# Kernel optimization log

Measured on AMD Instinct MI355X. Metric: run time of the kernel, lower is better.

The kernel has to match this reference:

```python
import jax, jax.numpy as jnp
import numpy as np


def setup_inputs() -> dict:
    key = jax.random.key(0)
    k1, k2, k3, k4, k5 = jax.random.split(key, 5)
    n_mol, n_atm, d_feat, n_props = 128, 64, 384, 64
    n_ref = n_mol * n_atm  # 8192 reference atoms (flattened)
    # element labels in {1,2,3,4} (e.g. H,C,N,O); all atoms nondummy (Z>0)
    Z_ref = jax.random.randint(k1, (n_mol, n_atm), 1, 5)
    Z = jax.random.randint(k2, (n_mol, n_atm), 1, 5)
    # descriptors, scaled so the poly kernel K^expK stays O(1)
    scale = 1.0 / np.sqrt(d_feat).astype(np.float32)
    X_ref = jax.random.normal(k3, (n_ref, d_feat), jnp.float32) * scale
    desc = jax.random.normal(k4, (n_mol, n_atm, d_feat), jnp.float32) * scale
    Alpha = jax.random.normal(k5, (n_props, n_ref), jnp.float32)
    return {"Alpha": Alpha, "X_ref": X_ref, "desc": desc,
            "Z_ref": Z_ref, "Z": Z, "expK": 2}


def reference(Alpha, X_ref, desc, Z_ref, Z, expK):
    # Faithful dense formulation of the per-element gather/matmul/scatter:
    # y[p, j] = sum_i Alpha[p, i] * (X_ref[i] . X_in[j])^expK * [Z_ref[i] == Z[j]]
    # Each query atom j belongs to exactly one element, so the masked dense
    # kernel reproduces the grouped computation exactly (same flat ordering
    # as torch's molecule-major concatenation).
    d_feat = X_ref.shape[-1]
    X_in = desc.reshape(-1, d_feat)                      # [N_in, d]
    K = jnp.power(X_ref @ X_in.T, expK)                  # [N_ref, N_in]
    mask = Z_ref.reshape(-1)[:, None] == Z.reshape(-1)[None, :]
    y = Alpha @ jnp.where(mask, K, jnp.float32(0.0))     # [n_props, N_in]
    return y
```

## Files before the change

### kernel.cpp

```cpp
#include <hip/hip_runtime.h>
#include <hip/hip_bf16.h>
#include <stdint.h>


typedef __attribute__((ext_vector_type(8))) short bf16x8;
typedef __attribute__((ext_vector_type(4))) float f32x4;
typedef __attribute__((ext_vector_type(4))) unsigned int u32x4;

#define DFEAT  384
#define NREF   8192
#define NIN    8192
#define NPROPS 64
#define BJ 128
#define BI 128
#define BK 64
#define KSTEPS (DFEAT / BK)
#define CAP    8704
#define NSTRIP (CAP / BJ)

__device__ __forceinline__ void gload_lds16(const void* g, void* l) {
  __builtin_amdgcn_global_load_lds(
      (const __attribute__((address_space(1))) void*)g,
      (__attribute__((address_space(3))) void*)l,
      16, 0, 0);
}

__device__ __forceinline__ unsigned short bfbits(float f) {
  __hip_bfloat16 h = __float2bfloat16(f);
  return __builtin_bit_cast(unsigned short, h);
}

__device__ __forceinline__ float pwr(float s, int expK) {
  if (expK == 2) return s * s;
  float r = 1.0f;
  for (int e = 0; e < expK; ++e) r *= s;
  return r;
}

__global__ __launch_bounds__(256) void partition2_kernel(
    const int* __restrict__ Za, const int* __restrict__ Zb,
    int* __restrict__ perma, int* __restrict__ permb,
    int* __restrict__ goffa, int* __restrict__ goffb) {
  const int* Zin = blockIdx.x ? Zb : Za;
  int* perm = blockIdx.x ? permb : perma;
  int* goff = blockIdx.x ? goffb : goffa;

  __shared__ int cnt[256][4];
  __shared__ int gstart[4];
  __shared__ int gtot[4];
  const int t = threadIdx.x;
  const int base = t * 32;

  int c[4] = {0, 0, 0, 0};
  int zloc[32];
  #pragma unroll
  for (int e = 0; e < 32; ++e) {
    zloc[e] = (Zin[base + e] - 1) & 3;
    ++c[zloc[e]];
  }
  #pragma unroll
  for (int b = 0; b < 4; ++b) cnt[t][b] = c[b];
  __syncthreads();

  const int w = t >> 6, l = t & 63;
  {
    int v0 = cnt[4 * l + 0][w], v1 = cnt[4 * l + 1][w];
    int v2 = cnt[4 * l + 2][w], v3 = cnt[4 * l + 3][w];
    int s = v0 + v1 + v2 + v3;
    int inc = s;
    #pragma unroll
    for (int d = 1; d < 64; d <<= 1) {
      int o = __shfl_up(inc, d, 64);
      if (l >= d) inc += o;
    }
    const int excl = inc - s;
    cnt[4 * l + 0][w] = excl;
    cnt[4 * l + 1][w] = excl + v0;
    cnt[4 * l + 2][w] = excl + v0 + v1;
    cnt[4 * l + 3][w] = excl + v0 + v1 + v2;
    if (l == 63) gtot[w] = inc;
  }
  __syncthreads();

  if (t == 0) {
    int off = 0;
    #pragma unroll
    for (int b = 0; b < 4; ++b) {
      gstart[b] = off; goff[b] = off;
      off += ((gtot[b] + 127) >> 7) << 7;
    }
    goff[4] = off;
  }
  __syncthreads();

  for (int s = t; s < CAP; s += 256) perm[s] = -1;
  __syncthreads();

  int pos[4];
  #pragma unroll
  for (int b = 0; b < 4; ++b) pos[b] = gstart[b] + cnt[t][b];
  #pragma unroll
  for (int e = 0; e < 32; ++e) {
    const int z = zloc[e];
    perm[pos[z]++] = base + e;
  }
}

#define XSEC (CAP * (DFEAT / 4) / 256)
__global__ void gather_all(const float* __restrict__ Xr_in,
                           const float* __restrict__ Xi_in,
                           const float* __restrict__ Al_in,
                           const int* __restrict__ perm_i,
                           const int* __restrict__ perm_j,
                           __hip_bfloat16* __restrict__ Xr_g,
                           __hip_bfloat16* __restrict__ Xi_g,
                           __hip_bfloat16* __restrict__ Ab_g) {
  const int b = blockIdx.x;
  if (b < 2 * XSEC) {
    const bool isA = (b < XSEC);
    const float* in = isA ? Xr_in : Xi_in;
    const int* perm = isA ? perm_i : perm_j;
    __hip_bfloat16* out = isA ? Xr_g : Xi_g;
    const int idx = (isA ? b : b - XSEC) * 256 + threadIdx.x;
    const int per_row = DFEAT / 4;
    const int slot = idx / per_row;
    const int c4 = (idx % per_row) * 4;
    const int src = perm[slot];
    ushort4 o = make_ushort4(0, 0, 0, 0);
    if (src >= 0) {
      float4 v = *reinterpret_cast<const float4*>(in + (size_t)src * DFEAT + c4);
      o.x = bfbits(v.x); o.y = bfbits(v.y); o.z = bfbits(v.z); o.w = bfbits(v.w);
    }
    *reinterpret_cast<ushort4*>(out + (size_t)slot * DFEAT + c4) = o;
  } else {
    const int t = (b - 2 * XSEC) * 256 + threadIdx.x;
    const int per_row = CAP / 4;
    const int p  = t / per_row;
    const int c4 = t % per_row;
    const int blk = c4 >> 3;
    const int g   = c4 & 7;
    const int l4g = g >> 1;
    const int eh  = g & 1;
    ushort4 o;
    unsigned short* op = &o.x;
    #pragma unroll
    for (int r = 0; r < 4; ++r) {
      const int slot = blk * 32 + eh * 16 + l4g * 4 + r;
      const int src = perm_i[slot];
      op[r] = (src >= 0) ? bfbits(Al_in[(size_t)p * NREF + src]) : (unsigned short)0;
    }
    *reinterpret_cast<ushort4*>(Ab_g + (size_t)p * CAP + blk * 32 + l4g * 8 + eh * 4) = o;
  }
}

__global__ void reduce_scatter(const float* __restrict__ partial,
                               const int* __restrict__ permj,
                               float* __restrict__ out, int nsplit) {
  const int idx = blockIdx.x * blockDim.x + threadIdx.x;
  const int p = idx / CAP;
  const int slot = idx % CAP;
  const int dst = permj[slot];
  if (dst < 0) return;
  float s = 0.f;
  for (int sp = 0; sp < nsplit; ++sp)
    s += partial[(size_t)sp * NPROPS * CAP + (size_t)p * CAP + slot];
  out[(size_t)p * NIN + dst] = s;
}

__global__ __launch_bounds__(256, 2) void fused_poly_kernel(
    const __hip_bfloat16* __restrict__ Xr,
    const __hip_bfloat16* __restrict__ Xi,
    const __hip_bfloat16* __restrict__ Abp,
    const int* __restrict__ ioff,
    const int* __restrict__ joff,
    const int* __restrict__ expKp,
    float* __restrict__ partial,
    int nsplit, int chunk)
{
  const int flat = blockIdx.x;
  const int newflat = (flat & 7) * chunk + (flat >> 3);
  const int strip = newflat / nsplit;
  const int split = newflat % nsplit;
  const int j0 = strip * BJ;

  if (j0 >= joff[4]) return;

  int grp = 0;
  grp += (j0 >= joff[1]);
  grp += (j0 >= joff[2]);
  grp += (j0 >= joff[3]);
  const int ibase = ioff[grp];
  const int ntiles_g = (ioff[grp + 1] - ibase) / BI;

  const int tb = ntiles_g / nsplit;
  const int rem = ntiles_g % nsplit;
  const int ntiles = tb + (split < rem ? 1 : 0);
  const int tile_begin = split * tb + (split < rem ? split : rem);

  const int tid  = threadIdx.x;
  const int wid  = tid >> 6;
  const int lane = tid & 63;
  const int l15  = lane & 15;
  const int l4   = lane >> 4;
  const int s7   = l15 & 7;
  const int wi   = wid >> 1;
  const int wj   = wid & 1;

  __shared__ alignas(16) __hip_bfloat16 lA[2][BI * BK];
  __shared__ alignas(16) __hip_bfloat16 lB[2][BJ * BK];

  const int expK = *expKp;

  const int srow = lane >> 3;
  const int scol = ((lane & 7) ^ srow) * 8;

  auto stage = [&](int buf, int i0s, int kks) {
    #pragma unroll
    for (int q = 0; q < 4; ++q) {
      const int c = wid * 4 + q;
      const int grow = c * 8 + srow;
      const size_t gc = (size_t)kks * BK + scol;
      gload_lds16(Xr + (size_t)(i0s + grow) * DFEAT + gc, &lA[buf][c * 512]);
      gload_lds16(Xi + (size_t)(j0  + grow) * DFEAT + gc, &lB[buf][c * 512]);
    }
  };

  f32x4 accO[4][4];
  #pragma unroll
  for (int a = 0; a < 4; ++a)
    #pragma unroll
    for (int n = 0; n < 4; ++n)
      accO[a][n] = (f32x4){0.f, 0.f, 0.f, 0.f};

  if (ntiles > 0) {
    int cur = 0;
    stage(0, ibase + tile_begin * BI, 0);

    for (int t = 0; t < ntiles; ++t) {
      const int i0 = ibase + (tile_begin + t) * BI;

      f32x4 acc[4][4];
      #pragma unroll
      for (int m = 0; m < 4; ++m)
        #pragma unroll
        for (int n = 0; n < 4; ++n)
          acc[m][n] = (f32x4){0.f, 0.f, 0.f, 0.f};

      for (int kk = 0; kk < KSTEPS; ++kk) {
        bool staged = true;
        if (kk < KSTEPS - 1) {
          stage(cur ^ 1, i0, kk + 1);
        } else if (t < ntiles - 1) {
          stage(cur ^ 1, i0 + BI, 0);
        } else {
          staged = false;
        }
        if (staged) asm volatile("s_waitcnt vmcnt(8)" ::: "memory");
        else        asm volatile("s_waitcnt vmcnt(0)" ::: "memory");
        __builtin_amdgcn_s_barrier();

        __builtin_amdgcn_s_setprio(1);
        #pragma unroll
        for (int kap = 0; kap < 2; ++kap) {
          bf16x8 aF[4], bF[4];
          #pragma unroll
          for (int m = 0; m < 4; ++m) {
            const int rA = wi * 64 + m * 16 + l15;
            aF[m] = *reinterpret_cast<const bf16x8*>(
                (char*)(&lA[cur][0]) + rA * 128 + (((kap * 4 + l4) ^ s7) << 4));
          }
          #pragma unroll
          for (int n = 0; n < 4; ++n) {
            const int rB = wj * 64 + n * 16 + l15;
            bF[n] = *reinterpret_cast<const bf16x8*>(
                (char*)(&lB[cur][0]) + rB * 128 + (((kap * 4 + l4) ^ s7) << 4));
          }
          #pragma unroll
          for (int m = 0; m < 4; ++m)
            #pragma unroll
            for (int n = 0; n < 4; ++n)
              acc[m][n] = __builtin_amdgcn_mfma_f32_16x16x32_bf16(
                  aF[m], bF[n], acc[m][n], 0, 0, 0);
        }
        __builtin_amdgcn_s_setprio(0);
        asm volatile("s_waitcnt lgkmcnt(0)" ::: "memory");
        __builtin_amdgcn_s_barrier();
        cur ^= 1;
      }

      bf16x8 aP[2][4];
      #pragma unroll
      for (int ks = 0; ks < 2; ++ks)
        #pragma unroll
        for (int a = 0; a < 4; ++a)
          aP[ks][a] = *reinterpret_cast<const bf16x8*>(
              Abp + (size_t)(a * 16 + l15) * CAP + i0 + wi * 64 + ks * 32 + l4 * 8);

      uint32_t lov[4][4], hiv[4][4];
      #pragma unroll
      for (int m = 0; m < 4; ++m) {
        #pragma unroll
        for (int n = 0; n < 4; ++n) {
          const float p0 = pwr(acc[m][n][0], expK);
          const float p1 = pwr(acc[m][n][1], expK);
          const float p2 = pwr(acc[m][n][2], expK);
          const float p3 = pwr(acc[m][n][3], expK);
          lov[m][n] = (uint32_t)bfbits(p0) | ((uint32_t)bfbits(p1) << 16);
          hiv[m][n] = (uint32_t)bfbits(p2) | ((uint32_t)bfbits(p3) << 16);
        }
      }

      __builtin_amdgcn_s_setprio(1);
      #pragma unroll
      for (int ks = 0; ks < 2; ++ks) {
        #pragma unroll
        for (int n = 0; n < 4; ++n) {
          u32x4 tw;
          tw[0] = lov[2 * ks][n];
          tw[1] = hiv[2 * ks][n];
          tw[2] = lov[2 * ks + 1][n];
          tw[3] = hiv[2 * ks + 1][n];
          const bf16x8 bP = __builtin_bit_cast(bf16x8, tw);
          #pragma unroll
          for (int a = 0; a < 4; ++a)
            accO[a][n] = __builtin_amdgcn_mfma_f32_16x16x32_bf16(
                aP[ks][a], bP, accO[a][n], 0, 0, 0);
        }
      }
      __builtin_amdgcn_s_setprio(0);
    }
  }

  float* rb = (float*)lA;
  if (wi == 1) {
    #pragma unroll
    for (int a = 0; a < 4; ++a)
      #pragma unroll
      for (int n = 0; n < 4; ++n)
        #pragma unroll
        for (int r = 0; r < 4; ++r)
          rb[wj * 4096 + (a * 16 + l4 * 4 + r) * 64 + n * 16 + l15] =
              accO[a][n][r];
  }
  __syncthreads();
  if (wi == 0) {
    float* po = partial + (size_t)split * NPROPS * CAP;
    #pragma unroll
    for (int a = 0; a < 4; ++a)
      #pragma unroll
      for (int n = 0; n < 4; ++n)
        #pragma unroll
        for (int r = 0; r < 4; ++r) {
          const int p = a * 16 + l4 * 4 + r;
          const int jl = wj * 64 + n * 16 + l15;
          po[(size_t)p * CAP + j0 + jl] =
              accO[a][n][r] + rb[wj * 4096 + p * 64 + n * 16 + l15];
        }
  }
}

extern "C" void kernel_launch(void* const* d_in, const int* in_sizes, int n_in,
                              void* d_out, int out_size, void* d_ws, size_t ws_size,
                              hipStream_t stream) {
  (void)in_sizes; (void)n_in; (void)out_size;
  const float* Alpha = (const float*)d_in[0];
  const float* X_ref = (const float*)d_in[1];
  const float* desc  = (const float*)d_in[2];
  const int*   Z_ref = (const int*)d_in[3];
  const int*   Z     = (const int*)d_in[4];
  const int*   expK  = (const int*)d_in[5];
  float* out = (float*)d_out;

  char* ws = (char*)d_ws;
  size_t off = 0;
  auto alloc = [&](size_t b) { void* p = ws + off; off = (off + b + 255) & ~255ULL; return p; };

  int* perm_i = (int*)alloc(CAP * 4);
  int* perm_j = (int*)alloc(CAP * 4);
  int* ioff   = (int*)alloc(8 * 4);
  int* joff   = (int*)alloc(8 * 4);
  __hip_bfloat16* Xr_g = (__hip_bfloat16*)alloc((size_t)CAP * DFEAT * 2);
  __hip_bfloat16* Xi_g = (__hip_bfloat16*)alloc((size_t)CAP * DFEAT * 2);
  __hip_bfloat16* Ab_g = (__hip_bfloat16*)alloc((size_t)NPROPS * CAP * 2);

  int nsplit = 8;
  while (nsplit > 1 && off + (size_t)nsplit * NPROPS * CAP * 4 > ws_size) nsplit >>= 1;
  float* partial = (float*)alloc((size_t)nsplit * NPROPS * CAP * 4);

  partition2_kernel<<<dim3(2), 256, 0, stream>>>(
      Z_ref, Z, perm_i, perm_j, ioff, joff);

  gather_all<<<dim3(2 * XSEC + NPROPS * (CAP / 4) / 256), 256, 0, stream>>>(
      X_ref, desc, Alpha, perm_i, perm_j, Xr_g, Xi_g, Ab_g);

  const int grid = NSTRIP * nsplit;
  fused_poly_kernel<<<dim3(grid), 256, 0, stream>>>(
      Xr_g, Xi_g, Ab_g, ioff, joff, expK, partial, nsplit, grid / 8);

  reduce_scatter<<<dim3(NPROPS * CAP / 256), 256, 0, stream>>>(
      partial, perm_j, out, nsplit);
}
```

Before: 77.67 us.

## Drop LDS staging and load MFMA operands directly from global memory

```diff
diff --git a/kernel.cpp b/kernel.cpp
--- a/kernel.cpp
+++ b/kernel.cpp
@@ -13,17 +13,9 @@
 #define NPROPS 64
 #define BJ 128
 #define BI 128
-#define BK 64
-#define KSTEPS (DFEAT / BK)
+#define KSTEPS 6
 #define CAP    8704
 #define NSTRIP (CAP / BJ)
-
-__device__ __forceinline__ void gload_lds16(const void* g, void* l) {
-  __builtin_amdgcn_global_load_lds(
-      (const __attribute__((address_space(1))) void*)g,
-      (__attribute__((address_space(3))) void*)l,
-      16, 0, 0);
-}
 
 __device__ __forceinline__ unsigned short bfbits(float f) {
   __hip_bfloat16 h = __float2bfloat16(f);
@@ -167,7 +159,7 @@
   out[(size_t)p * NIN + dst] = s;
 }
 
-__global__ __launch_bounds__(256, 2) void fused_poly_kernel(
+__global__ __launch_bounds__(256, 4) void fused_poly_kernel(
     const __hip_bfloat16* __restrict__ Xr,
     const __hip_bfloat16* __restrict__ Xi,
     const __hip_bfloat16* __restrict__ Abp,
@@ -182,7 +174,6 @@
   const int strip = newflat / nsplit;
   const int split = newflat % nsplit;
   const int j0 = strip * BJ;
-
   if (j0 >= joff[4]) return;
 
   int grp = 0;
@@ -191,7 +182,6 @@
   grp += (j0 >= joff[3]);
   const int ibase = ioff[grp];
   const int ntiles_g = (ioff[grp + 1] - ibase) / BI;
-
   const int tb = ntiles_g / nsplit;
   const int rem = ntiles_g % nsplit;
   const int ntiles = tb + (split < rem ? 1 : 0);
@@ -202,90 +192,54 @@
   const int lane = tid & 63;
   const int l15  = lane & 15;
   const int l4   = lane >> 4;
-  const int s7   = l15 & 7;
-  const int wi   = wid >> 1;
-  const int wj   = wid & 1;
-
-  __shared__ alignas(16) __hip_bfloat16 lA[2][BI * BK];
-  __shared__ alignas(16) __hip_bfloat16 lB[2][BJ * BK];
+  const int jw   = j0 + wid * 32;
 
   const int expK = *expKp;
 
-  const int srow = lane >> 3;
-  const int scol = ((lane & 7) ^ srow) * 8;
-
-  auto stage = [&](int buf, int i0s, int kks) {
-    #pragma unroll
-    for (int q = 0; q < 4; ++q) {
-      const int c = wid * 4 + q;
-      const int grow = c * 8 + srow;
-      const size_t gc = (size_t)kks * BK + scol;
-      gload_lds16(Xr + (size_t)(i0s + grow) * DFEAT + gc, &lA[buf][c * 512]);
-      gload_lds16(Xi + (size_t)(j0  + grow) * DFEAT + gc, &lB[buf][c * 512]);
-    }
-  };
-
-  f32x4 accO[4][4];
+  const __hip_bfloat16* xiB = Xi + (size_t)(jw + l15) * DFEAT + l4 * 8;
+
+  f32x4 accO[4][2];
   #pragma unroll
   for (int a = 0; a < 4; ++a)
     #pragma unroll
-    for (int n = 0; n < 4; ++n)
+    for (int n = 0; n < 2; ++n)
       accO[a][n] = (f32x4){0.f, 0.f, 0.f, 0.f};
 
-  if (ntiles > 0) {
-    int cur = 0;
-    stage(0, ibase + tile_begin * BI, 0);
-
-    for (int t = 0; t < ntiles; ++t) {
-      const int i0 = ibase + (tile_begin + t) * BI;
-
-      f32x4 acc[4][4];
+  #pragma unroll 1
+  for (int t = 0; t < ntiles; ++t) {
+    const int i0 = ibase + (tile_begin + t) * BI;
+
+    #pragma unroll 1
+    for (int h = 0; h < 2; ++h) {
+      const __hip_bfloat16* xrA =
+          Xr + (size_t)(i0 + h * 64 + l15) * DFEAT + l4 * 8;
+
+      f32x4 acc[4][2];
       #pragma unroll
       for (int m = 0; m < 4; ++m)
         #pragma unroll
-        for (int n = 0; n < 4; ++n)
+        for (int n = 0; n < 2; ++n)
           acc[m][n] = (f32x4){0.f, 0.f, 0.f, 0.f};
 
+      #pragma unroll
       for (int kk = 0; kk < KSTEPS; ++kk) {
-        bool staged = true;
-        if (kk < KSTEPS - 1) {
-          stage(cur ^ 1, i0, kk + 1);
-        } else if (t < ntiles - 1) {
-          stage(cur ^ 1, i0 + BI, 0);
-        } else {
-          staged = false;
-        }
-        if (staged) asm volatile("s_waitcnt vmcnt(8)" ::: "memory");
-        else        asm volatile("s_waitcnt vmcnt(0)" ::: "memory");
-        __builtin_amdgcn_s_barrier();
-
-        __builtin_amdgcn_s_setprio(1);
         #pragma unroll
         for (int kap = 0; kap < 2; ++kap) {
-          bf16x8 aF[4], bF[4];
+          const int co = kk * 64 + kap * 32;
+          bf16x8 aF[4], bF[2];
           #pragma unroll
-          for (int m = 0; m < 4; ++m) {
-            const int rA = wi * 64 + m * 16 + l15;
-            aF[m] = *reinterpret_cast<const bf16x8*>(
-                (char*)(&lA[cur][0]) + rA * 128 + (((kap * 4 + l4) ^ s7) << 4));
-          }
+          for (int m = 0; m < 4; ++m)
+            aF[m] = *reinterpret_cast<const bf16x8*>(xrA + m * (16 * DFEAT) + co);
           #pragma unroll
-          for (int n = 0; n < 4; ++n) {
-            const int rB = wj * 64 + n * 16 + l15;
-            bF[n] = *reinterpret_cast<const bf16x8*>(
-                (char*)(&lB[cur][0]) + rB * 128 + (((kap * 4 + l4) ^ s7) << 4));
-          }
+          for (int n = 0; n < 2; ++n)
+            bF[n] = *reinterpret_cast<const bf16x8*>(xiB + n * (16 * DFEAT) + co);
           #pragma unroll
           for (int m = 0; m < 4; ++m)
             #pragma unroll
-            for (int n = 0; n < 4; ++n)
+            for (int n = 0; n < 2; ++n)
               acc[m][n] = __builtin_amdgcn_mfma_f32_16x16x32_bf16(
                   aF[m], bF[n], acc[m][n], 0, 0, 0);
         }
-        __builtin_amdgcn_s_setprio(0);
-        asm volatile("s_waitcnt lgkmcnt(0)" ::: "memory");
-        __builtin_amdgcn_s_barrier();
-        cur ^= 1;
       }
 
       bf16x8 aP[2][4];
@@ -294,13 +248,13 @@
         #pragma unroll
         for (int a = 0; a < 4; ++a)
           aP[ks][a] = *reinterpret_cast<const bf16x8*>(
-              Abp + (size_t)(a * 16 + l15) * CAP + i0 + wi * 64 + ks * 32 + l4 * 8);
-
-      uint32_t lov[4][4], hiv[4][4];
+              Abp + (size_t)(a * 16 + l15) * CAP + i0 + h * 64 + ks * 32 + l4 * 8);
+
+      uint32_t lov[4][2], hiv[4][2];
       #pragma unroll
       for (int m = 0; m < 4; ++m) {
         #pragma unroll
-        for (int n = 0; n < 4; ++n) {
+        for (int n = 0; n < 2; ++n) {
           const float p0 = pwr(acc[m][n][0], expK);
           const float p1 = pwr(acc[m][n][1], expK);
           const float p2 = pwr(acc[m][n][2], expK);
@@ -310,11 +264,10 @@
         }
       }
 
-      __builtin_amdgcn_s_setprio(1);
       #pragma unroll
       for (int ks = 0; ks < 2; ++ks) {
         #pragma unroll
-        for (int n = 0; n < 4; ++n) {
+        for (int n = 0; n < 2; ++n) {
           u32x4 tw;
           tw[0] = lov[2 * ks][n];
           tw[1] = hiv[2 * ks][n];
@@ -327,36 +280,19 @@
                 aP[ks][a], bP, accO[a][n], 0, 0, 0);
         }
       }
-      __builtin_amdgcn_s_setprio(0);
-    }
-  }
-
-  float* rb = (float*)lA;
-  if (wi == 1) {
-    #pragma unroll
-    for (int a = 0; a < 4; ++a)
-      #pragma unroll
-      for (int n = 0; n < 4; ++n)
-        #pragma unroll
-        for (int r = 0; r < 4; ++r)
-          rb[wj * 4096 + (a * 16 + l4 * 4 + r) * 64 + n * 16 + l15] =
-              accO[a][n][r];
-  }
-  __syncthreads();
-  if (wi == 0) {
-    float* po = partial + (size_t)split * NPROPS * CAP;
-    #pragma unroll
-    for (int a = 0; a < 4; ++a)
-      #pragma unroll
-      for (int n = 0; n < 4; ++n)
-        #pragma unroll
-        for (int r = 0; r < 4; ++r) {
-          const int p = a * 16 + l4 * 4 + r;
-          const int jl = wj * 64 + n * 16 + l15;
-          po[(size_t)p * CAP + j0 + jl] =
-              accO[a][n][r] + rb[wj * 4096 + p * 64 + n * 16 + l15];
-        }
-  }
+    }
+  }
+
+  float* po = partial + (size_t)split * NPROPS * CAP;
+  #pragma unroll
+  for (int a = 0; a < 4; ++a)
+    #pragma unroll
+    for (int n = 0; n < 2; ++n)
+      #pragma unroll
+      for (int r = 0; r < 4; ++r) {
+        const int p = a * 16 + l4 * 4 + r;
+        po[(size_t)p * CAP + jw + n * 16 + l15] = accO[a][n][r];
+      }
 }
 
 extern "C" void kernel_launch(void* const* d_in, const int* in_sizes, int n_in,
```

After: 201.1 us. 159% more time.
